# Performance work log

Measured on AMD Instinct MI355X. Metric: run time of the kernel, lower is better.

The kernel has to match this reference:

```python
import jax, jax.numpy as jnp
import numpy as np

SEQ, BATCH = 2048, 32
ENC_HS, DEC_HS = 512, 1024

def setup_inputs() -> dict:
    key = jax.random.key(0)
    k1, k2, k3, k4, k5 = jax.random.split(key, 5)
    return {
        "hidden": jax.random.normal(k1, (BATCH, DEC_HS), dtype=jnp.float32),
        "encoder_outputs": jax.random.normal(k2, (SEQ, BATCH, 2 * ENC_HS), dtype=jnp.float32),
        "attn_w": jax.random.normal(k3, (2 * ENC_HS + DEC_HS, DEC_HS), dtype=jnp.float32) * 0.02,
        "attn_b": jax.random.normal(k4, (DEC_HS,), dtype=jnp.float32) * 0.02,
        "v": jax.random.normal(k5, (DEC_HS,), dtype=jnp.float32),
    }

def reference(hidden, encoder_outputs, attn_w, attn_b, v):
    # encoder_outputs: [S, B, 2*enc_hs] -> [B, S, 2*enc_hs]
    enc = jnp.transpose(encoder_outputs, (1, 0, 2))
    B, S, _ = enc.shape
    # hidden: [B, dec_hs] broadcast to [B, S, dec_hs]
    h = jnp.broadcast_to(hidden[:, None, :], (B, S, hidden.shape[-1]))
    cat = jnp.concatenate([h, enc], axis=2)            # [B, S, 2*enc_hs+dec_hs]
    energy = jnp.tanh(cat @ attn_w + attn_b)            # [B, S, dec_hs]
    scores = jnp.einsum("bsd,d->bs", energy, v)        # [B, S]
    return jax.nn.softmax(scores, axis=1)
```

## Files before the change

kernel.cpp:

```cpp
#include <hip/hip_runtime.h>


typedef _Float16 f16;
typedef _Float16 half8 __attribute__((ext_vector_type(8)));
typedef float f32x4 __attribute__((ext_vector_type(4)));

#define KDIM 1024
#define SEQ  2048
#define MROWS 65536

typedef __attribute__((address_space(1))) void gvoid;
typedef __attribute__((address_space(3))) void svoid;

__device__ __forceinline__ void gload_lds16(const void* g, void* l) {
    __builtin_amdgcn_global_load_lds((const gvoid*)g, (svoid*)l, 16, 0, 0);
}

__global__ __launch_bounds__(256) void prep_w(const float* __restrict__ w,
                                              f16* __restrict__ wt) {
    int idx  = blockIdx.x * 256 + threadIdx.x;
    int kblk = idx & 3;
    int nloc = (idx >> 2) & 127;
    int tk   = idx >> 9;
    int ks   = tk & 31, nq = tk >> 5;
    int n_g  = nq * 128 + nloc;
    int kb   = 1024 + ks * 32 + kblk * 8;
    half8 h;
#pragma unroll
    for (int j = 0; j < 8; ++j)
        h[j] = (f16)w[(size_t)(kb + j) * 1024 + n_g];
    int p = nloc * 4 + ((kblk + (nloc >> 1)) & 3);
    *(half8*)&wt[(size_t)tk * 4096 + p * 8] = h;
}

__global__ __launch_bounds__(256) void prep_hb(const float* __restrict__ hidden,
                                               const float* __restrict__ attn_w,
                                               const float* __restrict__ attn_b,
                                               float* __restrict__ hb) {
    int b = blockIdx.x >> 2;
    int n = (blockIdx.x & 3) * 256 + threadIdx.x;
    const float* h = hidden + (size_t)b * 1024;
    float acc = attn_b[n];
#pragma unroll 8
    for (int k = 0; k < 1024; ++k)
        acc += h[k] * attn_w[(size_t)k * 1024 + n];
    hb[(size_t)b * 1024 + n] = acc;
}

__global__ __launch_bounds__(256, 3)
void fused_energy(const float* __restrict__ enc, const f16* __restrict__ wt,
                  const float* __restrict__ hb, const float* __restrict__ vvec,
                  float* __restrict__ partout) {
    __shared__ f16 Bls[2][4096];
    __shared__ f16 Als[4096];
    __shared__ float red[2][128];

    const int tid  = threadIdx.x;
    const int lane = tid & 63;
    const int wv   = tid >> 6;
    const int wm   = wv >> 1;
    const int wn   = wv & 1;
    const int l15  = lane & 15;
    const int l4   = lane >> 4;

    const int bid   = blockIdx.x;
    const int xcd   = bid & 7;
    const int chunk = bid >> 3;
    const int mt    = xcd * 64 + (chunk >> 3);
    const int nq    = chunk & 7;
    const int mrow0 = mt * 128;
    const int ncol0 = nq * 128;

    const char* wtNq = (const char*)wt + (size_t)nq * 32 * 8192;

    const int arow = tid >> 1;
    const int akh  = tid & 1;
    const float* aG = enc + (size_t)(mrow0 + arow) * KDIM + akh * 16;
    const int pw0 = arow * 4 + ((akh * 2     + (arow >> 1)) & 3);
    const int pw1 = arow * 4 + ((akh * 2 + 1 + (arow >> 1)) & 3);

    int aOffB[4], bOffB[4];
#pragma unroll
    for (int mi = 0; mi < 4; ++mi) {
        int r = wm * 64 + mi * 16 + l15;
        aOffB[mi] = (r * 4 + ((l4 + (r >> 1)) & 3)) * 16;
    }
#pragma unroll
    for (int nj = 0; nj < 4; ++nj) {
        int n = wn * 64 + nj * 16 + l15;
        bOffB[nj] = (n * 4 + ((l4 + (n >> 1)) & 3)) * 16;
    }

    const f32x4 zero = {0.f, 0.f, 0.f, 0.f};
    f32x4 acc[4][4];
#pragma unroll
    for (int mi = 0; mi < 4; ++mi)
#pragma unroll
        for (int nj = 0; nj < 4; ++nj) acc[mi][nj] = zero;

    f32x4 rA[4];
    half8 bf[4], af[4];

#define WAITV(N) asm volatile("s_waitcnt vmcnt(" #N ")" ::: "memory")
#define LGKM0    asm volatile("s_waitcnt lgkmcnt(0)" ::: "memory")
#define BAR      __builtin_amdgcn_s_barrier()

#define STAGE_B(KS)                                                           \
    {                                                                         \
        const char* s_ = wtNq + (size_t)(KS) * 8192 + tid * 16;               \
        char* d_ = (char*)&Bls[(KS) & 1][0] + tid * 16;                       \
        gload_lds16(s_, d_);                                                  \
        gload_lds16(s_ + 4096, d_ + 4096);                                    \
    }
#define LOADA(KS)                                                             \
    {                                                                         \
        const float* p_ = aG + (KS) * 32;                                     \
        rA[0] = *(const f32x4*)(p_);      rA[1] = *(const f32x4*)(p_ + 4);    \
        rA[2] = *(const f32x4*)(p_ + 8);  rA[3] = *(const f32x4*)(p_ + 12);   \
    }
#define CVTA()                                                                \
    {                                                                         \
        half8 h0_, h1_;                                                       \
        _Pragma("unroll") for (int j = 0; j < 4; ++j) {                       \
            h0_[j] = (f16)rA[0][j]; h0_[4 + j] = (f16)rA[1][j];               \
            h1_[j] = (f16)rA[2][j]; h1_[4 + j] = (f16)rA[3][j];               \
        }                                                                     \
        *(half8*)((char*)Als + pw0 * 16) = h0_;                               \
        *(half8*)((char*)Als + pw1 * 16) = h1_;                               \
    }
#define COMPUTE(KS)                                                           \
    {                                                                         \
        const char* bb_ = (const char*)&Bls[(KS) & 1][0];                     \
        _Pragma("unroll") for (int nj = 0; nj < 4; ++nj)                      \
            bf[nj] = *(const half8*)(bb_ + bOffB[nj]);                        \
        _Pragma("unroll") for (int mi = 0; mi < 4; ++mi)                      \
            af[mi] = *(const half8*)((char*)Als + aOffB[mi]);                 \
        LGKM0;                                                                \
        __builtin_amdgcn_s_setprio(1);                                        \
        _Pragma("unroll") for (int mi = 0; mi < 4; ++mi)                      \
            _Pragma("unroll") for (int nj = 0; nj < 4; ++nj)                  \
                acc[mi][nj] = __builtin_amdgcn_mfma_f32_16x16x32_f16(         \
                    af[mi], bf[nj], acc[mi][nj], 0, 0, 0);                    \
        __builtin_amdgcn_s_setprio(0);                                        \
    }

    LOADA(0);
    STAGE_B(0);

    for (int ks = 0; ks < 31; ++ks) {
        LGKM0;
        BAR;
        WAITV(2);
        CVTA();
        LOADA(ks + 1);
        STAGE_B(ks + 1);
        WAITV(6);
        LGKM0;
        BAR;
        COMPUTE(ks);
    }
    LGKM0;
    BAR;
    WAITV(2);
    CVTA();
    WAITV(0);
    LGKM0;
    BAR;
    COMPUTE(31);

#undef STAGE_B
#undef LOADA
#undef CVTA
#undef COMPUTE

    float vv[4];
#pragma unroll
    for (int nj = 0; nj < 4; ++nj)
        vv[nj] = vvec[ncol0 + wn * 64 + nj * 16 + l15];
#pragma unroll
    for (int mi = 0; mi < 4; ++mi) {
#pragma unroll
        for (int rg = 0; rg < 4; ++rg) {
            int rl = wm * 64 + mi * 16 + l4 * 4 + rg;
            const float* hbrow = hb + (size_t)((mrow0 + rl) & 31) * 1024
                                 + ncol0 + wn * 64 + l15;
            float sum = 0.f;
#pragma unroll
            for (int nj = 0; nj < 4; ++nj) {
                float e  = acc[mi][nj][rg] + hbrow[nj * 16];
                float e2 = __expf(2.f * e);
                sum += (1.f - 2.f / (e2 + 1.f)) * vv[nj];
            }
            float p = sum;
            p += __shfl_xor(p, 1);
            p += __shfl_xor(p, 2);
            p += __shfl_xor(p, 4);
            p += __shfl_xor(p, 8);
            if (l15 == 0) red[wn][rl] = p;
        }
    }
    __syncthreads();
    if (tid < 128) {
        float s = red[0][tid] + red[1][tid];
        partout[(size_t)nq * MROWS + mrow0 + tid] = s;
    }
}

__global__ __launch_bounds__(256) void softmax_rows(const float* __restrict__ part,
                                                    float* __restrict__ out) {
    const int b = blockIdx.x;
    const int tid  = threadIdx.x;
    const int lane = tid & 63;
    const int wv   = tid >> 6;
    __shared__ float sred[4];
    __shared__ float ssum[4];
    float x[8];
    float mx = -3.4e38f;
#pragma unroll
    for (int j = 0; j < 8; ++j) {
        int flat = (tid + j * 256) * 32 + b;
        float v = 0.f;
#pragma unroll
        for (int q = 0; q < 8; ++q) v += part[(size_t)q * MROWS + flat];
        x[j] = v;
        mx = fmaxf(mx, v);
    }
#pragma unroll
    for (int o = 1; o < 64; o <<= 1) mx = fmaxf(mx, __shfl_xor(mx, o));
    if (lane == 0) sred[wv] = mx;
    __syncthreads();
    mx = fmaxf(fmaxf(sred[0], sred[1]), fmaxf(sred[2], sred[3]));
    float s = 0.f;
#pragma unroll
    for (int j = 0; j < 8; ++j) { x[j] = __expf(x[j] - mx); s += x[j]; }
#pragma unroll
    for (int o = 1; o < 64; o <<= 1) s += __shfl_xor(s, o);
    if (lane == 0) ssum[wv] = s;
    __syncthreads();
    s = ssum[0] + ssum[1] + ssum[2] + ssum[3];
    float inv = 1.f / s;
#pragma unroll
    for (int j = 0; j < 8; ++j) out[(size_t)b * SEQ + tid + j * 256] = x[j] * inv;
}

extern "C" void kernel_launch(void* const* d_in, const int* in_sizes, int n_in,
                              void* d_out, int out_size, void* d_ws, size_t ws_size,
                              hipStream_t stream) {
    const float* hidden = (const float*)d_in[0];
    const float* enc    = (const float*)d_in[1];
    const float* attn_w = (const float*)d_in[2];
    const float* attn_b = (const float*)d_in[3];
    const float* v      = (const float*)d_in[4];
    float* out = (float*)d_out;

    f16*   wt   = (f16*)d_ws;
    float* hb   = (float*)((char*)d_ws + 2097152);
    float* part = (float*)((char*)d_ws + 2097152 + 131072);

    prep_w<<<512, 256, 0, stream>>>(attn_w, wt);
    prep_hb<<<128, 256, 0, stream>>>(hidden, attn_w, attn_b, hb);
    fused_energy<<<4096, 256, 0, stream>>>(enc, wt, hb, v, part);
    softmax_rows<<<32, 256, 0, stream>>>(part, out);
}
```

Before: 295.5 us.

## Stage fp32 A tiles directly into LDS with double buffering

Replaces the register-staged A path (global load, convert to f16, write to LDS) with direct global_load_lds DMA of raw fp32 encoder rows into a swizzled, double-buffered LDS area. The f16 conversion now happens after the LDS read, just before the MFMAs. The loop becomes a simple one-barrier double-buffer pipeline in which the next tile is staged while the current one is computed. This removes VGPR staging and the fine-grained waitcnt choreography, but it doubles LDS footprint and read traffic for A and moves the conversion into the compute phase.

```diff
diff --git a/kernel.cpp b/kernel.cpp
--- a/kernel.cpp
+++ b/kernel.cpp
@@ -51,8 +51,8 @@
 void fused_energy(const float* __restrict__ enc, const f16* __restrict__ wt,
                   const float* __restrict__ hb, const float* __restrict__ vvec,
                   float* __restrict__ partout) {
-    __shared__ f16 Bls[2][4096];
-    __shared__ f16 Als[4096];
+    __shared__ char AlsA[2][16384];
+    __shared__ char AlsB[2][8192];
     __shared__ float red[2][128];
 
     const int tid  = threadIdx.x;
@@ -73,18 +73,31 @@
 
     const char* wtNq = (const char*)wt + (size_t)nq * 32 * 8192;
 
-    const int arow = tid >> 1;
-    const int akh  = tid & 1;
-    const float* aG = enc + (size_t)(mrow0 + arow) * KDIM + akh * 16;
-    const int pw0 = arow * 4 + ((akh * 2     + (arow >> 1)) & 3);
-    const int pw1 = arow * 4 + ((akh * 2 + 1 + (arow >> 1)) & 3);
-
-    int aOffB[4], bOffB[4];
+    const float* aSrc[4];
+    int aDst[4];
+#pragma unroll
+    for (int i = 0; i < 4; ++i) {
+        int s    = i * 256 + tid;
+        int r    = s >> 3;
+        int h    = s & 7;
+        int pos  = h >> 1;
+        int half = h & 1;
+        int g    = pos ^ (r & 3);
+        int sh   = half ^ ((r >> 2) & 1);
+        aSrc[i] = enc + (size_t)(mrow0 + r) * KDIM + g * 8 + sh * 4;
+        aDst[i] = s * 16;
+    }
+
+    int aLo[4], aHi[4];
 #pragma unroll
     for (int mi = 0; mi < 4; ++mi) {
-        int r = wm * 64 + mi * 16 + l15;
-        aOffB[mi] = (r * 4 + ((l4 + (r >> 1)) & 3)) * 16;
-    }
+        int r   = wm * 64 + mi * 16 + l15;
+        int bse = r * 128 + ((l4 ^ (r & 3)) * 32);
+        int hb_ = (r >> 2) & 1;
+        aLo[mi] = bse + hb_ * 16;
+        aHi[mi] = bse + (1 - hb_) * 16;
+    }
+    int bOffB[4];
 #pragma unroll
     for (int nj = 0; nj < 4; ++nj) {
         int n = wn * 64 + nj * 16 + l15;
@@ -98,44 +111,33 @@
 #pragma unroll
         for (int nj = 0; nj < 4; ++nj) acc[mi][nj] = zero;
 
-    f32x4 rA[4];
-    half8 bf[4], af[4];
-
-#define WAITV(N) asm volatile("s_waitcnt vmcnt(" #N ")" ::: "memory")
-#define LGKM0    asm volatile("s_waitcnt lgkmcnt(0)" ::: "memory")
-#define BAR      __builtin_amdgcn_s_barrier()
-
-#define STAGE_B(KS)                                                           \
+#define STAGE(KS, BUF)                                                        \
     {                                                                         \
-        const char* s_ = wtNq + (size_t)(KS) * 8192 + tid * 16;               \
-        char* d_ = (char*)&Bls[(KS) & 1][0] + tid * 16;                       \
-        gload_lds16(s_, d_);                                                  \
-        gload_lds16(s_ + 4096, d_ + 4096);                                    \
-    }
-#define LOADA(KS)                                                             \
+        char* da_ = AlsA[BUF];                                                \
+        _Pragma("unroll") for (int i = 0; i < 4; ++i)                         \
+            gload_lds16(aSrc[i] + (KS) * 32, da_ + aDst[i]);                  \
+        const char* sb_ = wtNq + (size_t)(KS) * 8192 + tid * 16;              \
+        char* db_ = AlsB[BUF] + tid * 16;                                     \
+        gload_lds16(sb_, db_);                                                \
+        gload_lds16(sb_ + 4096, db_ + 4096);                                  \
+    }
+#define COMPUTE(BUF)                                                          \
     {                                                                         \
-        const float* p_ = aG + (KS) * 32;                                     \
-        rA[0] = *(const f32x4*)(p_);      rA[1] = *(const f32x4*)(p_ + 4);    \
-        rA[2] = *(const f32x4*)(p_ + 8);  rA[3] = *(const f32x4*)(p_ + 12);   \
-    }
-#define CVTA()                                                                \
-    {                                                                         \
-        half8 h0_, h1_;                                                       \
-        _Pragma("unroll") for (int j = 0; j < 4; ++j) {                       \
-            h0_[j] = (f16)rA[0][j]; h0_[4 + j] = (f16)rA[1][j];               \
-            h1_[j] = (f16)rA[2][j]; h1_[4 + j] = (f16)rA[3][j];               \
+        const char* ab_ = AlsA[BUF];                                          \
+        const char* bb_ = AlsB[BUF];                                          \
+        f32x4 alo[4], ahi[4];                                                 \
+        half8 bf[4], af[4];                                                   \
+        _Pragma("unroll") for (int mi = 0; mi < 4; ++mi) {                    \
+            alo[mi] = *(const f32x4*)(ab_ + aLo[mi]);                         \
+            ahi[mi] = *(const f32x4*)(ab_ + aHi[mi]);                         \
         }                                                                     \
-        *(half8*)((char*)Als + pw0 * 16) = h0_;                               \
-        *(half8*)((char*)Als + pw1 * 16) = h1_;                               \
-    }
-#define COMPUTE(KS)                                                           \
-    {                                                                         \
-        const char* bb_ = (const char*)&Bls[(KS) & 1][0];                     \
         _Pragma("unroll") for (int nj = 0; nj < 4; ++nj)                      \
             bf[nj] = *(const half8*)(bb_ + bOffB[nj]);                        \
         _Pragma("unroll") for (int mi = 0; mi < 4; ++mi)                      \
-            af[mi] = *(const half8*)((char*)Als + aOffB[mi]);                 \
-        LGKM0;                                                                \
+            _Pragma("unroll") for (int j = 0; j < 4; ++j) {                   \
+                af[mi][j]     = (f16)alo[mi][j];                              \
+                af[mi][4 + j] = (f16)ahi[mi][j];                              \
+            }                                                                 \
         __builtin_amdgcn_s_setprio(1);                                        \
         _Pragma("unroll") for (int mi = 0; mi < 4; ++mi)                      \
             _Pragma("unroll") for (int nj = 0; nj < 4; ++nj)                  \
@@ -144,33 +146,18 @@
         __builtin_amdgcn_s_setprio(0);                                        \
     }
 
-    LOADA(0);
-    STAGE_B(0);
-
+    STAGE(0, 0);
+    __syncthreads();
+
+#pragma unroll 2
     for (int ks = 0; ks < 31; ++ks) {
-        LGKM0;
-        BAR;
-        WAITV(2);
-        CVTA();
-        LOADA(ks + 1);
-        STAGE_B(ks + 1);
-        WAITV(6);
-        LGKM0;
-        BAR;
-        COMPUTE(ks);
-    }
-    LGKM0;
-    BAR;
-    WAITV(2);
-    CVTA();
-    WAITV(0);
-    LGKM0;
-    BAR;
-    COMPUTE(31);
-
-#undef STAGE_B
-#undef LOADA
-#undef CVTA
+        STAGE(ks + 1, (ks & 1) ^ 1);
+        COMPUTE(ks & 1);
+        __syncthreads();
+    }
+    COMPUTE(1);
+
+#undef STAGE
 #undef COMPUTE
 
     float vv[4];
```

New measurement: 317.0 us. 7.3% more time.
